# Kernel optimization log

Measured on AMD Instinct MI355X. Metric: run time of the kernel, lower is better.

## Reference

```python
import jax, jax.numpy as jnp
import numpy as np

B, T, I, H, C = 8192, 784, 1, 30, 10


def setup_inputs() -> dict:
    key = jax.random.key(0)
    ks = jax.random.split(key, 7)
    s_ih = 1.0 / np.sqrt(H)
    return {
        "x": jax.random.normal(ks[0], (B, T, I), dtype=jnp.float32),
        "W_ih": jax.random.uniform(ks[1], (H, I), jnp.float32, -s_ih, s_ih),
        "W_hh": jax.random.uniform(ks[2], (H, H), jnp.float32, -s_ih, s_ih),
        "b_ih": jax.random.uniform(ks[3], (H,), jnp.float32, -s_ih, s_ih),
        "b_hh": jax.random.uniform(ks[4], (H,), jnp.float32, -s_ih, s_ih),
        "W_fc": jax.random.uniform(ks[5], (C, H), jnp.float32, -s_ih, s_ih),
        "b_fc": jax.random.uniform(ks[6], (C,), jnp.float32, -s_ih, s_ih),
    }


def reference(x, W_ih, W_hh, b_ih, b_hh, W_fc, b_fc):
    # x: [B, T, I] -> scan over time. h_t = tanh(x_t W_ih^T + b_ih + h W_hh^T + b_hh)
    xs = jnp.swapaxes(x, 0, 1)  # [T, B, I]
    h0 = jnp.zeros((x.shape[0], W_hh.shape[0]), dtype=x.dtype)
    bias = b_ih + b_hh  # [H]

    def step(h, xt):
        h_new = jnp.tanh(xt @ W_ih.T + h @ W_hh.T + bias)
        return h_new, None

    hT, _ = jax.lax.scan(step, h0, xs)  # hT: [B, H] == out[:, -1, :]
    return hT @ W_fc.T + b_fc  # [B, C]
```

## Files before the change

### kernel.cpp

```cpp
#include <hip/hip_runtime.h>


#define BB 8192
#define TT 784
#define HH 30
#define HP 32
#define CC 10
#define TPB 16
#define ROWS 2
#define NB 16
#define LSTR 36

__global__ __launch_bounds__(256, 2)
void rnn_scan_kernel(const float* __restrict__ x,
                     const float* __restrict__ W_ih,
                     const float* __restrict__ W_hh,
                     const float* __restrict__ b_ih,
                     const float* __restrict__ b_hh,
                     const float* __restrict__ W_fc,
                     const float* __restrict__ b_fc,
                     float* __restrict__ out) {
    __shared__ float hbuf[NB * LSTR];

    const int tid = threadIdx.x;
    const int bl  = tid >> 4;
    const int r   = tid & 15;
    const int i0  = r * ROWS;
    const int b   = blockIdx.x * NB + bl;

    float w[ROWS][HP];
    float bias[ROWS], wih[ROWS];
#pragma unroll
    for (int rr = 0; rr < ROWS; ++rr) {
        const int i = i0 + rr;
        const bool valid = (i < HH);
#pragma unroll
        for (int j = 0; j < HP; ++j)
            w[rr][j] = (valid && (j < HH)) ? W_hh[i * HH + j] : 0.0f;
        bias[rr] = valid ? (b_ih[i] + b_hh[i]) : 0.0f;
        wih[rr]  = valid ? W_ih[i] : 0.0f;
    }

    float* hp = &hbuf[bl * LSTR];
    *(float2*)&hp[i0] = make_float2(0.f, 0.f);
    __builtin_amdgcn_wave_barrier();

    const float* xb = x + (size_t)b * TT;
    float4 xq = *(const float4*)(xb);

    for (int q = 0; q < TT / 4; ++q) {
        float4 nxt = (q + 1 < TT / 4) ? *(const float4*)(xb + (q + 1) * 4)
                                      : make_float4(0.f, 0.f, 0.f, 0.f);
#pragma unroll
        for (int u = 0; u < 4; ++u) {
            const float xt = (u == 0) ? xq.x : (u == 1) ? xq.y
                           : (u == 2) ? xq.z : xq.w;
            float a0 = bias[0] + xt * wih[0], a0b = 0.f;
            float a1 = bias[1] + xt * wih[1], a1b = 0.f;
#pragma unroll
            for (int jq = 0; jq < HP / 4; ++jq) {
                const float4 hq = *(const float4*)(hp + jq * 4);
                a0  += w[0][jq * 4 + 0] * hq.x;
                a0b += w[0][jq * 4 + 1] * hq.y;
                a0  += w[0][jq * 4 + 2] * hq.z;
                a0b += w[0][jq * 4 + 3] * hq.w;
                a1  += w[1][jq * 4 + 0] * hq.x;
                a1b += w[1][jq * 4 + 1] * hq.y;
                a1  += w[1][jq * 4 + 2] * hq.z;
                a1b += w[1][jq * 4 + 3] * hq.w;
            }
            const float acc0 = a0 + a0b;
            const float acc1 = a1 + a1b;
            float2 hn;
            hn.x = 1.0f - 2.0f * __builtin_amdgcn_rcpf(__expf(2.0f * acc0) + 1.0f);
            hn.y = 1.0f - 2.0f * __builtin_amdgcn_rcpf(__expf(2.0f * acc1) + 1.0f);
            __builtin_amdgcn_wave_barrier();
            *(float2*)&hp[i0] = hn;
            __builtin_amdgcn_wave_barrier();
        }
        xq = nxt;
    }

    if (r < CC) {
        const int c = r;
        float acc = b_fc[c];
#pragma unroll
        for (int j = 0; j < HH; ++j)
            acc += W_fc[c * HH + j] * hp[j];
        out[(size_t)b * CC + c] = acc;
    }
}

extern "C" void kernel_launch(void* const* d_in, const int* in_sizes, int n_in,
                              void* d_out, int out_size, void* d_ws, size_t ws_size,
                              hipStream_t stream) {
    const float* x    = (const float*)d_in[0];
    const float* W_ih = (const float*)d_in[1];
    const float* W_hh = (const float*)d_in[2];
    const float* b_ih = (const float*)d_in[3];
    const float* b_hh = (const float*)d_in[4];
    const float* W_fc = (const float*)d_in[5];
    const float* b_fc = (const float*)d_in[6];

    hipLaunchKernelGGL(rnn_scan_kernel,
                       dim3(BB / NB), dim3(NB * TPB), 0, stream,
                       x, W_ih, W_hh, b_ih, b_hh, W_fc, b_fc,
                       (float*)d_out);
}
```

Measured before the change: 291.3 us.

## Map one hidden row per thread with 32 threads per batch element

Each thread now computes a single hidden unit rather than two, so a batch element uses 32 lanes and a block holds 8 elements, and launch bounds ask for 4 blocks per CU. This shortens the serial per-step FMA chain and the register footprint, trading more threads and more LDS broadcast reads per step for that. Tanh now uses exp2 with a folded constant and explicit FMAs.

Measured after the change: 334.5 us. +14.8%, slower.

```diff
diff --git a/kernel.cpp b/kernel.cpp
--- a/kernel.cpp
+++ b/kernel.cpp
@@ -1,17 +1,15 @@
 #include <hip/hip_runtime.h>
 
 
-#define BB 8192
 #define TT 784
 #define HH 30
 #define HP 32
 #define CC 10
-#define TPB 16
-#define ROWS 2
-#define NB 16
+#define TPB 32
+#define NB 8
 #define LSTR 36
 
-__global__ __launch_bounds__(256, 2)
+__global__ __launch_bounds__(256, 4)
 void rnn_scan_kernel(const float* __restrict__ x,
                      const float* __restrict__ W_ih,
                      const float* __restrict__ W_hh,
@@ -23,26 +21,20 @@
     __shared__ float hbuf[NB * LSTR];
 
     const int tid = threadIdx.x;
-    const int bl  = tid >> 4;
-    const int r   = tid & 15;
-    const int i0  = r * ROWS;
+    const int bl  = tid >> 5;
+    const int r   = tid & 31;
     const int b   = blockIdx.x * NB + bl;
 
-    float w[ROWS][HP];
-    float bias[ROWS], wih[ROWS];
+    float w[HP];
+    const bool valid = (r < HH);
 #pragma unroll
-    for (int rr = 0; rr < ROWS; ++rr) {
-        const int i = i0 + rr;
-        const bool valid = (i < HH);
-#pragma unroll
-        for (int j = 0; j < HP; ++j)
-            w[rr][j] = (valid && (j < HH)) ? W_hh[i * HH + j] : 0.0f;
-        bias[rr] = valid ? (b_ih[i] + b_hh[i]) : 0.0f;
-        wih[rr]  = valid ? W_ih[i] : 0.0f;
-    }
+    for (int j = 0; j < HP; ++j)
+        w[j] = (valid && (j < HH)) ? W_hh[r * HH + j] : 0.0f;
+    const float bias = valid ? (b_ih[r] + b_hh[r]) : 0.0f;
+    const float wih  = valid ? W_ih[r] : 0.0f;
 
     float* hp = &hbuf[bl * LSTR];
-    *(float2*)&hp[i0] = make_float2(0.f, 0.f);
+    hp[r] = 0.0f;
     __builtin_amdgcn_wave_barrier();
 
     const float* xb = x + (size_t)b * TT;
@@ -55,39 +47,33 @@
         for (int u = 0; u < 4; ++u) {
             const float xt = (u == 0) ? xq.x : (u == 1) ? xq.y
                            : (u == 2) ? xq.z : xq.w;
-            float a0 = bias[0] + xt * wih[0], a0b = 0.f;
-            float a1 = bias[1] + xt * wih[1], a1b = 0.f;
+            float a0 = __builtin_fmaf(xt, wih, bias);
+            float a1 = 0.0f;
 #pragma unroll
             for (int jq = 0; jq < HP / 4; ++jq) {
                 const float4 hq = *(const float4*)(hp + jq * 4);
-                a0  += w[0][jq * 4 + 0] * hq.x;
-                a0b += w[0][jq * 4 + 1] * hq.y;
-                a0  += w[0][jq * 4 + 2] * hq.z;
-                a0b += w[0][jq * 4 + 3] * hq.w;
-                a1  += w[1][jq * 4 + 0] * hq.x;
-                a1b += w[1][jq * 4 + 1] * hq.y;
-                a1  += w[1][jq * 4 + 2] * hq.z;
-                a1b += w[1][jq * 4 + 3] * hq.w;
+                a0 = __builtin_fmaf(w[jq * 4 + 0], hq.x, a0);
+                a1 = __builtin_fmaf(w[jq * 4 + 1], hq.y, a1);
+                a0 = __builtin_fmaf(w[jq * 4 + 2], hq.z, a0);
+                a1 = __builtin_fmaf(w[jq * 4 + 3], hq.w, a1);
             }
-            const float acc0 = a0 + a0b;
-            const float acc1 = a1 + a1b;
-            float2 hn;
-            hn.x = 1.0f - 2.0f * __builtin_amdgcn_rcpf(__expf(2.0f * acc0) + 1.0f);
-            hn.y = 1.0f - 2.0f * __builtin_amdgcn_rcpf(__expf(2.0f * acc1) + 1.0f);
+            const float acc = a0 + a1;
+            const float e  = __builtin_exp2f(acc * 2.885390081777927f);
+            const float hn = __builtin_fmaf(-2.0f,
+                                 __builtin_amdgcn_rcpf(e + 1.0f), 1.0f);
             __builtin_amdgcn_wave_barrier();
-            *(float2*)&hp[i0] = hn;
+            hp[r] = hn;
             __builtin_amdgcn_wave_barrier();
         }
         xq = nxt;
     }
 
     if (r < CC) {
-        const int c = r;
-        float acc = b_fc[c];
+        float acc = b_fc[r];
 #pragma unroll
         for (int j = 0; j < HH; ++j)
-            acc += W_fc[c * HH + j] * hp[j];
-        out[(size_t)b * CC + c] = acc;
+            acc = __builtin_fmaf(W_fc[r * HH + j], hp[j], acc);
+        out[(size_t)b * CC + r] = acc;
     }
 }
 
@@ -103,7 +89,7 @@
     const float* b_fc = (const float*)d_in[6];
 
     hipLaunchKernelGGL(rnn_scan_kernel,
-                       dim3(BB / NB), dim3(NB * TPB), 0, stream,
+                       dim3(8192 / NB), dim3(NB * TPB), 0, stream,
                        x, W_ih, W_hh, b_ih, b_hh, W_fc, b_fc,
                        (float*)d_out);
 }
```
